# Performance work log

Hardware: AMD Instinct MI355X
Metric: run time of the kernel (lower is better)

Reference implementation:

```python
import jax, jax.numpy as jnp
import numpy as np

N_NODES = 50000
N_EDGES = 800000
D_IN = 256
D_OUT = 128


def setup_inputs() -> dict:
    key = jax.random.key(0)
    k1, k2, k3 = jax.random.split(key, 3)
    x = jax.random.normal(k1, (N_NODES, D_IN), dtype=jnp.float32)
    edge_index = jax.random.randint(k2, (2, N_EDGES), 0, N_NODES, dtype=jnp.int64)
    W = jax.random.normal(k3, (D_IN, D_OUT), dtype=jnp.float32) / np.sqrt(D_IN)
    b = jnp.zeros((D_OUT,), dtype=jnp.float32)
    prelu_a = jnp.full((D_OUT,), 0.25, dtype=jnp.float32)  # PyTorch PReLU default init
    return {"x": x, "edge_index": edge_index, "W": W, "b": b, "prelu_a": prelu_a}


def reference(x, edge_index, W, b, prelu_a):
    N = x.shape[0]
    # GCNConv default: add self-loops, symmetric deg^{-1/2} normalization
    self_loops = jnp.arange(N, dtype=edge_index.dtype)
    src = jnp.concatenate([edge_index[0], self_loops])  # message source j
    dst = jnp.concatenate([edge_index[1], self_loops])  # aggregation target i
    deg = jax.ops.segment_sum(jnp.ones_like(dst, dtype=x.dtype), dst, num_segments=N)
    dinv = jnp.where(deg > 0, jax.lax.rsqrt(deg), 0.0)
    norm = dinv[src] * dinv[dst]  # [E+N]
    h = x @ W  # [N, D_OUT] linear transform before aggregation
    msg = h[src] * norm[:, None]  # gather + scale
    out = jax.ops.segment_sum(msg, dst, num_segments=N) + b  # scatter-add + bias
    # per-channel PReLU
    return jnp.where(out > 0, out, prelu_a * out)
```

## Files before the change

kernel.cpp:

```cpp
#include <hip/hip_runtime.h>

#define N_NODES 50000
#define N_EDGES 800000
#define D_IN    256
#define D_OUT   128
#define ELL_S   64
#define PART_BLKS 391
#define GEMM_BLKS 391
#define NBINS   196
#define EPB     2048
#define CAPB    40

typedef __attribute__((ext_vector_type(8))) short short8;
typedef __attribute__((ext_vector_type(4))) float floatx4;

__device__ __forceinline__ unsigned short f2bf(float f) {
    unsigned int u = __float_as_uint(f);
    unsigned int r = (u + 0x7fffu + ((u >> 16) & 1u)) >> 16;
    return (unsigned short)r;
}
__device__ __forceinline__ unsigned int pack2(float a, float b) {
    return (unsigned int)f2bf(a) | ((unsigned int)f2bf(b) << 16);
}
__device__ __forceinline__ float bfl(unsigned int u) { return __uint_as_float(u << 16); }
__device__ __forceinline__ float bfh(unsigned int u) { return __uint_as_float(u & 0xffff0000u); }

__global__ __launch_bounds__(256) void fused_kernel(const float* __restrict__ x,
                                                    const float* __restrict__ W,
                                                    const void* __restrict__ ei,
                                                    int* __restrict__ packed,
                                                    int* __restrict__ blkBinCnt,
                                                    unsigned short* __restrict__ h) {
    __shared__ unsigned short As[128][40];
    __shared__ unsigned short bLds[4096 * 8];
    __shared__ int hist[NBINS];
    __shared__ int found32;
    const int bid = blockIdx.x;
    const int tid = threadIdx.x;

    if (bid < PART_BLKS) {
        int sb = bid;
        if (tid < NBINS) hist[tid] = 0;
        if (tid == 0) found32 = 0;
        __syncthreads();
        {
            const unsigned int* e32 = (const unsigned int*)ei;
            if (e32[2 * tid + 1] != 0u) atomicOr(&found32, 1);
        }
        __syncthreads();
        int is64 = !found32;

        int ebase = sb * EPB + tid;
        int sv[8], bn[8], dl[8], lr[8];
        if (is64) {
            const long long* p = (const long long*)ei;
#pragma unroll
            for (int i = 0; i < 8; i++) {
                int e = ebase + i * 256;
                if (e < N_EDGES) {
                    sv[i] = (int)p[e];
                    int d = (int)p[N_EDGES + e];
                    bn[i] = d >> 8; dl[i] = d & 255;
                } else bn[i] = -1;
            }
        } else {
            const int* p = (const int*)ei;
#pragma unroll
            for (int i = 0; i < 8; i++) {
                int e = ebase + i * 256;
                if (e < N_EDGES) {
                    sv[i] = p[e];
                    int d = p[N_EDGES + e];
                    bn[i] = d >> 8; dl[i] = d & 255;
                } else bn[i] = -1;
            }
        }
#pragma unroll
        for (int i = 0; i < 8; i++)
            if (bn[i] >= 0) lr[i] = atomicAdd(&hist[bn[i]], 1);
#pragma unroll
        for (int i = 0; i < 8; i++) {
            if (bn[i] >= 0 && lr[i] < CAPB)
                packed[((size_t)sb * NBINS + bn[i]) * CAPB + lr[i]] = sv[i] | (dl[i] << 24);
        }
        __syncthreads();
        for (int t = tid; t < NBINS; t += 256)
            blkBinCnt[sb * NBINS + t] = hist[t];
        return;
    }

#pragma unroll
    for (int seg = 0; seg < 16; seg++) {
        int g = seg * 256 + tid;
        int gl = g & 63;
        int kc = (g >> 6) & 7;
        int ct = g >> 9;
        int n  = ct * 16 + (gl & 15);
        int kb = kc * 32 + ((gl >> 4) & 3) * 8;
        unsigned int p[4];
#pragma unroll
        for (int jj = 0; jj < 4; jj++) {
            float a = W[(size_t)(kb + 2 * jj + 0) * D_OUT + n];
            float b = W[(size_t)(kb + 2 * jj + 1) * D_OUT + n];
            p[jj] = pack2(a, b);
        }
        *(uint4*)&bLds[(size_t)g * 8] = make_uint4(p[0], p[1], p[2], p[3]);
    }

    int row0 = (bid - PART_BLKS) * 128;
    int w    = tid >> 6;
    int lane = tid & 63;
    int quad = lane >> 4;
    int l15  = lane & 15;

    floatx4 acc[2][8];
#pragma unroll
    for (int i = 0; i < 2; i++)
#pragma unroll
        for (int j = 0; j < 8; j++) acc[i][j] = (floatx4){0.f, 0.f, 0.f, 0.f};

    int srow  = tid >> 1;
    int shalf = (tid & 1) * 16;
    const float* xrow = x + (size_t)(row0 + srow) * D_IN;
    bool svalid = (row0 + srow) < N_NODES;

    for (int k0 = 0; k0 < D_IN; k0 += 32) {
        uint4 p0 = make_uint4(0, 0, 0, 0), p1 = make_uint4(0, 0, 0, 0);
        if (svalid) {
            const float* src = xrow + k0 + shalf;
            float4 f0 = *(const float4*)(src + 0);
            float4 f1 = *(const float4*)(src + 4);
            float4 f2 = *(const float4*)(src + 8);
            float4 f3 = *(const float4*)(src + 12);
            p0 = make_uint4(pack2(f0.x, f0.y), pack2(f0.z, f0.w),
                            pack2(f1.x, f1.y), pack2(f1.z, f1.w));
            p1 = make_uint4(pack2(f2.x, f2.y), pack2(f2.z, f2.w),
                            pack2(f3.x, f3.y), pack2(f3.z, f3.w));
        }
        __syncthreads();
        *(uint4*)&As[srow][shalf + 0] = p0;
        *(uint4*)&As[srow][shalf + 8] = p1;
        __syncthreads();

        short8 a0 = *(const short8*)&As[w * 32 + l15][quad * 8];
        short8 a1 = *(const short8*)&As[w * 32 + 16 + l15][quad * 8];
        int kc = k0 >> 5;
#pragma unroll
        for (int ct = 0; ct < 8; ct++) {
            short8 b = *(const short8*)&bLds[(size_t)(((ct * 8 + kc) * 64 + lane)) * 8];
            acc[0][ct] = __builtin_amdgcn_mfma_f32_16x16x32_bf16(a0, b, acc[0][ct], 0, 0, 0);
            acc[1][ct] = __builtin_amdgcn_mfma_f32_16x16x32_bf16(a1, b, acc[1][ct], 0, 0, 0);
        }
    }

#pragma unroll
    for (int rt = 0; rt < 2; rt++) {
        int grow0 = row0 + w * 32 + rt * 16 + quad * 4;
#pragma unroll
        for (int r = 0; r < 4; r++) {
            int grow = grow0 + r;
            if (grow < N_NODES) {
#pragma unroll
                for (int ct = 0; ct < 8; ct++) {
                    h[(size_t)grow * D_OUT + ct * 16 + l15] = f2bf(acc[rt][ct][r]);
                }
            }
        }
    }
}

__global__ __launch_bounds__(256) void ell_kernel(const int* __restrict__ packed,
                                                  const int* __restrict__ blkBinCnt,
                                                  int* __restrict__ cnt,
                                                  int* __restrict__ bucket) {
    __shared__ int c256[256];
    int j = blockIdx.x, tid = threadIdx.x;
    c256[tid] = 0;
    __syncthreads();
    for (int sb = tid; sb < PART_BLKS; sb += 256) {
        int c = blkBinCnt[sb * NBINS + j];
        if (c > CAPB) c = CAPB;
        const int* seg = packed + ((size_t)sb * NBINS + j) * CAPB;
        for (int r = 0; r < c; ++r) {
            int rec = seg[r];
            int dl  = ((unsigned int)rec) >> 24;
            int s   = rec & 0xFFFFFF;
            int pos = atomicAdd(&c256[dl], 1);
            if (pos < ELL_S) bucket[(size_t)((j << 8) + dl) * ELL_S + pos] = s;
        }
    }
    __syncthreads();
    int d = (j << 8) + tid;
    if (d < N_NODES) cnt[d] = c256[tid];
}

#define GACC(U, F)                                      \
    a0 += bfl(U.x) * (F); a1 += bfh(U.x) * (F);         \
    a2 += bfl(U.y) * (F); a3 += bfh(U.y) * (F);         \
    a4 += bfl(U.z) * (F); a5 += bfh(U.z) * (F);         \
    a6 += bfl(U.w) * (F); a7 += bfh(U.w) * (F);

#define GBODY(SS, WW, KB)                                                         \
    {                                                                             \
        int lim = wave_max - (KB);                                                \
        if (lim > 16) lim = 16;                                                   \
        for (int k = 0; k < lim; k += 4) {                                        \
            int   s0 = __shfl((SS), gk + k + 0), s1 = __shfl((SS), gk + k + 1);   \
            int   s2 = __shfl((SS), gk + k + 2), s3 = __shfl((SS), gk + k + 3);   \
            float f0 = __shfl((WW), gk + k + 0), f1 = __shfl((WW), gk + k + 1);   \
            float f2 = __shfl((WW), gk + k + 2), f3 = __shfl((WW), gk + k + 3);   \
            uint4 u0 = *(const uint4*)(h + (size_t)s0 * D_OUT + co);              \
            uint4 u1 = *(const uint4*)(h + (size_t)s1 * D_OUT + co);              \
            uint4 u2 = *(const uint4*)(h + (size_t)s2 * D_OUT + co);              \
            uint4 u3 = *(const uint4*)(h + (size_t)s3 * D_OUT + co);              \
            GACC(u0, f0); GACC(u1, f1); GACC(u2, f2); GACC(u3, f3);               \
        }                                                                         \
    }

__global__ __launch_bounds__(256) void gather_kernel(
    const unsigned short* __restrict__ h, const int* __restrict__ cnt,
    const int* __restrict__ bucket, const float* __restrict__ bias,
    const float* __restrict__ pa, float* __restrict__ out) {
    int wave = (int)((blockIdx.x * blockDim.x + threadIdx.x) >> 6);
    int lane = threadIdx.x & 63;
    int g  = lane >> 4;
    int l  = lane & 15;
    int gk = g << 4;
    int d  = wave * 4 + g;
    if (wave >= N_NODES / 4) return;

    int nraw = cnt[d];
    int n = nraw < ELL_S ? nraw : ELL_S;
    float di = rsqrtf((float)(nraw + 1));

    int co = l * 8;

    uint4 us = *(const uint4*)(h + (size_t)d * D_OUT + co);
    float sl = di * di;
    float a0 = bfl(us.x) * sl, a1 = bfh(us.x) * sl;
    float a2 = bfl(us.y) * sl, a3 = bfh(us.y) * sl;
    float a4 = bfl(us.z) * sl, a5 = bfh(us.z) * sl;
    float a6 = bfl(us.w) * sl, a7 = bfh(us.w) * sl;

    int db = d * ELL_S;
    int   s0v = 0,   s1v = 0,   s2v = 0,   s3v = 0;
    float w0v = 0.f, w1v = 0.f, w2v = 0.f, w3v = 0.f;
    if (l      < n) { s0v = bucket[db + l];      w0v = rsqrtf((float)(cnt[s0v] + 1)) * di; }
    if (l + 16 < n) { s1v = bucket[db + l + 16]; w1v = rsqrtf((float)(cnt[s1v] + 1)) * di; }
    if (l + 32 < n) { s2v = bucket[db + l + 32]; w2v = rsqrtf((float)(cnt[s2v] + 1)) * di; }
    if (l + 48 < n) { s3v = bucket[db + l + 48]; w3v = rsqrtf((float)(cnt[s3v] + 1)) * di; }

    int wave_max = n;
    { int t = __shfl_xor(wave_max, 16); wave_max = t > wave_max ? t : wave_max; }
    { int t = __shfl_xor(wave_max, 32); wave_max = t > wave_max ? t : wave_max; }

    if (wave_max > 0)  GBODY(s0v, w0v, 0)
    if (wave_max > 16) GBODY(s1v, w1v, 16)
    if (wave_max > 32) GBODY(s2v, w2v, 32)
    if (wave_max > 48) GBODY(s3v, w3v, 48)

    int c = l * 8;
    float4 b0 = *(const float4*)&bias[c];
    float4 b1 = *(const float4*)&bias[c + 4];
    float4 p0 = *(const float4*)&pa[c];
    float4 p1 = *(const float4*)&pa[c + 4];
    float4 o0, o1;
    o0.x = a0 + b0.x; o0.y = a1 + b0.y; o0.z = a2 + b0.z; o0.w = a3 + b0.w;
    o1.x = a4 + b1.x; o1.y = a5 + b1.y; o1.z = a6 + b1.z; o1.w = a7 + b1.w;
    o0.x = o0.x > 0.f ? o0.x : p0.x * o0.x;
    o0.y = o0.y > 0.f ? o0.y : p0.y * o0.y;
    o0.z = o0.z > 0.f ? o0.z : p0.z * o0.z;
    o0.w = o0.w > 0.f ? o0.w : p0.w * o0.w;
    o1.x = o1.x > 0.f ? o1.x : p1.x * o1.x;
    o1.y = o1.y > 0.f ? o1.y : p1.y * o1.y;
    o1.z = o1.z > 0.f ? o1.z : p1.z * o1.z;
    o1.w = o1.w > 0.f ? o1.w : p1.w * o1.w;
    *(float4*)&out[(size_t)d * D_OUT + c]     = o0;
    *(float4*)&out[(size_t)d * D_OUT + c + 4] = o1;
}

extern "C" void kernel_launch(void* const* d_in, const int* in_sizes, int n_in,
                              void* d_out, int out_size, void* d_ws, size_t ws_size,
                              hipStream_t stream) {
    const float* x  = (const float*)d_in[0];
    const void*  ei = d_in[1];
    const float* W  = (const float*)d_in[2];
    const float* b  = (const float*)d_in[3];
    const float* pa = (const float*)d_in[4];
    float* out = (float*)d_out;

    char* w = (char*)d_ws;
    int*   packed = (int*)w;    w += (size_t)PART_BLKS * NBINS * CAPB * 4;
    int*   bbc    = (int*)w;    w += (size_t)PART_BLKS * NBINS * 4;
    int*   cnt    = (int*)w;    w += (size_t)NBINS * 256 * 4;
    int*   bucket = (int*)w;    w += (size_t)N_NODES * ELL_S * 4;
    unsigned short* h = (unsigned short*)w; w += (size_t)N_NODES * D_OUT * 2;

    fused_kernel<<<PART_BLKS + GEMM_BLKS, 256, 0, stream>>>(x, W, ei, packed, bbc, h);
    ell_kernel<<<NBINS, 256, 0, stream>>>(packed, bbc, cnt, bucket);
    gather_kernel<<<(N_NODES / 4 * 64 + 255) / 256, 256, 0, stream>>>(h, cnt, bucket, b, pa, out);
}
```

Baseline: 170.0 us.

## Regroup stages: pack W once, overlap GEMM with ELL build, pipeline gather loads

The edge partition now shares a kernel with a one-time packing of W into bf16 MFMA fragments in global memory. The GEMM blocks then share a launch with the ELL bucket-building blocks, so the GEMM overlaps with bucket construction. This removes the 64KB per-block LDS copy of W, which may raise occupancy, and the GEMM now reads its B fragments straight from global/L2. The gather loop is rewritten as a fixed 16-wide software-pipelined section so more row loads are in flight, though it always does 16 shuffles/loads per section regardless of the actual count.

```diff
diff --git a/kernel.cpp b/kernel.cpp
--- a/kernel.cpp
+++ b/kernel.cpp
@@ -6,6 +6,7 @@
 #define D_OUT   128
 #define ELL_S   64
 #define PART_BLKS 391
+#define PACK_BLKS 16
 #define GEMM_BLKS 391
 #define NBINS   196
 #define EPB     2048
@@ -25,73 +26,18 @@
 __device__ __forceinline__ float bfl(unsigned int u) { return __uint_as_float(u << 16); }
 __device__ __forceinline__ float bfh(unsigned int u) { return __uint_as_float(u & 0xffff0000u); }
 
-__global__ __launch_bounds__(256) void fused_kernel(const float* __restrict__ x,
-                                                    const float* __restrict__ W,
-                                                    const void* __restrict__ ei,
-                                                    int* __restrict__ packed,
-                                                    int* __restrict__ blkBinCnt,
-                                                    unsigned short* __restrict__ h) {
-    __shared__ unsigned short As[128][40];
-    __shared__ unsigned short bLds[4096 * 8];
+__global__ __launch_bounds__(256) void part_kernel(const void* __restrict__ ei,
+                                                   const float* __restrict__ W,
+                                                   unsigned short* __restrict__ bfrag,
+                                                   int* __restrict__ packed,
+                                                   int* __restrict__ blkBinCnt) {
     __shared__ int hist[NBINS];
     __shared__ int found32;
     const int bid = blockIdx.x;
     const int tid = threadIdx.x;
 
-    if (bid < PART_BLKS) {
-        int sb = bid;
-        if (tid < NBINS) hist[tid] = 0;
-        if (tid == 0) found32 = 0;
-        __syncthreads();
-        {
-            const unsigned int* e32 = (const unsigned int*)ei;
-            if (e32[2 * tid + 1] != 0u) atomicOr(&found32, 1);
-        }
-        __syncthreads();
-        int is64 = !found32;
-
-        int ebase = sb * EPB + tid;
-        int sv[8], bn[8], dl[8], lr[8];
-        if (is64) {
-            const long long* p = (const long long*)ei;
-#pragma unroll
-            for (int i = 0; i < 8; i++) {
-                int e = ebase + i * 256;
-                if (e < N_EDGES) {
-                    sv[i] = (int)p[e];
-                    int d = (int)p[N_EDGES + e];
-                    bn[i] = d >> 8; dl[i] = d & 255;
-                } else bn[i] = -1;
-            }
-        } else {
-            const int* p = (const int*)ei;
-#pragma unroll
-            for (int i = 0; i < 8; i++) {
-                int e = ebase + i * 256;
-                if (e < N_EDGES) {
-                    sv[i] = p[e];
-                    int d = p[N_EDGES + e];
-                    bn[i] = d >> 8; dl[i] = d & 255;
-                } else bn[i] = -1;
-            }
-        }
-#pragma unroll
-        for (int i = 0; i < 8; i++)
-            if (bn[i] >= 0) lr[i] = atomicAdd(&hist[bn[i]], 1);
-#pragma unroll
-        for (int i = 0; i < 8; i++) {
-            if (bn[i] >= 0 && lr[i] < CAPB)
-                packed[((size_t)sb * NBINS + bn[i]) * CAPB + lr[i]] = sv[i] | (dl[i] << 24);
-        }
-        __syncthreads();
-        for (int t = tid; t < NBINS; t += 256)
-            blkBinCnt[sb * NBINS + t] = hist[t];
-        return;
-    }
-
-#pragma unroll
-    for (int seg = 0; seg < 16; seg++) {
-        int g = seg * 256 + tid;
+    if (bid >= PART_BLKS) {
+        int g = (bid - PART_BLKS) * 256 + tid;
         int gl = g & 63;
         int kc = (g >> 6) & 7;
         int ct = g >> 9;
@@ -104,10 +50,93 @@
             float b = W[(size_t)(kb + 2 * jj + 1) * D_OUT + n];
             p[jj] = pack2(a, b);
         }
-        *(uint4*)&bLds[(size_t)g * 8] = make_uint4(p[0], p[1], p[2], p[3]);
-    }
-
-    int row0 = (bid - PART_BLKS) * 128;
+        *(uint4*)&bfrag[(size_t)g * 8] = make_uint4(p[0], p[1], p[2], p[3]);
+        return;
+    }
+
+    int sb = bid;
+    if (tid < NBINS) hist[tid] = 0;
+    if (tid == 0) found32 = 0;
+    __syncthreads();
+    {
+        const unsigned int* e32 = (const unsigned int*)ei;
+        if (e32[2 * tid + 1] != 0u) atomicOr(&found32, 1);
+    }
+    __syncthreads();
+    int is64 = !found32;
+
+    int ebase = sb * EPB + tid;
+    int sv[8], bn[8], dl[8], lr[8];
+    if (is64) {
+        const long long* p = (const long long*)ei;
+#pragma unroll
+        for (int i = 0; i < 8; i++) {
+            int e = ebase + i * 256;
+            if (e < N_EDGES) {
+                sv[i] = (int)p[e];
+                int d = (int)p[N_EDGES + e];
+                bn[i] = d >> 8; dl[i] = d & 255;
+            } else bn[i] = -1;
+        }
+    } else {
+        const int* p = (const int*)ei;
+#pragma unroll
+        for (int i = 0; i < 8; i++) {
+            int e = ebase + i * 256;
+            if (e < N_EDGES) {
+                sv[i] = p[e];
+                int d = p[N_EDGES + e];
+                bn[i] = d >> 8; dl[i] = d & 255;
+            } else bn[i] = -1;
+        }
+    }
+#pragma unroll
+    for (int i = 0; i < 8; i++)
+        if (bn[i] >= 0) lr[i] = atomicAdd(&hist[bn[i]], 1);
+#pragma unroll
+    for (int i = 0; i < 8; i++) {
+        if (bn[i] >= 0 && lr[i] < CAPB)
+            packed[((size_t)sb * NBINS + bn[i]) * CAPB + lr[i]] = sv[i] | (dl[i] << 24);
+    }
+    __syncthreads();
+    for (int t = tid; t < NBINS; t += 256)
+        blkBinCnt[sb * NBINS + t] = hist[t];
+}
+
+__global__ __launch_bounds__(256) void fused_kernel(const float* __restrict__ x,
+                                                    const unsigned short* __restrict__ bf,
+                                                    unsigned short* __restrict__ h,
+                                                    const int* __restrict__ packed,
+                                                    const int* __restrict__ blkBinCnt,
+                                                    int* __restrict__ cnt,
+                                                    int* __restrict__ bucket) {
+    __shared__ unsigned short As[128][40];
+    __shared__ int c256[256];
+    int tid = threadIdx.x;
+
+    if (blockIdx.x >= GEMM_BLKS) {
+        int j = blockIdx.x - GEMM_BLKS;
+        c256[tid] = 0;
+        __syncthreads();
+        for (int sb = tid; sb < PART_BLKS; sb += 256) {
+            int c = blkBinCnt[sb * NBINS + j];
+            if (c > CAPB) c = CAPB;
+            const int* seg = packed + ((size_t)sb * NBINS + j) * CAPB;
+            for (int r = 0; r < c; ++r) {
+                int rec = seg[r];
+                int dl  = ((unsigned int)rec) >> 24;
+                int s   = rec & 0xFFFFFF;
+                int pos = atomicAdd(&c256[dl], 1);
+                if (pos < ELL_S) bucket[(size_t)((j << 8) + dl) * ELL_S + pos] = s;
+            }
+        }
+        __syncthreads();
+        int d = (j << 8) + tid;
+        if (d < N_NODES) cnt[d] = c256[tid];
+        return;
+    }
+
+    int row0 = blockIdx.x * 128;
     int w    = tid >> 6;
     int lane = tid & 63;
     int quad = lane >> 4;
@@ -147,7 +176,7 @@
         int kc = k0 >> 5;
 #pragma unroll
         for (int ct = 0; ct < 8; ct++) {
-            short8 b = *(const short8*)&bLds[(size_t)(((ct * 8 + kc) * 64 + lane)) * 8];
+            short8 b = *(const short8*)&bf[(size_t)(((ct * 8 + kc) * 64 + lane)) * 8];
             acc[0][ct] = __builtin_amdgcn_mfma_f32_16x16x32_bf16(a0, b, acc[0][ct], 0, 0, 0);
             acc[1][ct] = __builtin_amdgcn_mfma_f32_16x16x32_bf16(a1, b, acc[1][ct], 0, 0, 0);
         }
@@ -167,31 +196,6 @@
             }
         }
     }
-}
-
-__global__ __launch_bounds__(256) void ell_kernel(const int* __restrict__ packed,
-                                                  const int* __restrict__ blkBinCnt,
-                                                  int* __restrict__ cnt,
-                                                  int* __restrict__ bucket) {
-    __shared__ int c256[256];
-    int j = blockIdx.x, tid = threadIdx.x;
-    c256[tid] = 0;
-    __syncthreads();
-    for (int sb = tid; sb < PART_BLKS; sb += 256) {
-        int c = blkBinCnt[sb * NBINS + j];
-        if (c > CAPB) c = CAPB;
-        const int* seg = packed + ((size_t)sb * NBINS + j) * CAPB;
-        for (int r = 0; r < c; ++r) {
-            int rec = seg[r];
-            int dl  = ((unsigned int)rec) >> 24;
-            int s   = rec & 0xFFFFFF;
-            int pos = atomicAdd(&c256[dl], 1);
-            if (pos < ELL_S) bucket[(size_t)((j << 8) + dl) * ELL_S + pos] = s;
-        }
-    }
-    __syncthreads();
-    int d = (j << 8) + tid;
-    if (d < N_NODES) cnt[d] = c256[tid];
 }
 
 #define GACC(U, F)                                      \
@@ -200,21 +204,32 @@
     a4 += bfl(U.z) * (F); a5 += bfh(U.z) * (F);         \
     a6 += bfl(U.w) * (F); a7 += bfh(U.w) * (F);
 
-#define GBODY(SS, WW, KB)                                                         \
-    {                                                                             \
-        int lim = wave_max - (KB);                                                \
-        if (lim > 16) lim = 16;                                                   \
-        for (int k = 0; k < lim; k += 4) {                                        \
-            int   s0 = __shfl((SS), gk + k + 0), s1 = __shfl((SS), gk + k + 1);   \
-            int   s2 = __shfl((SS), gk + k + 2), s3 = __shfl((SS), gk + k + 3);   \
-            float f0 = __shfl((WW), gk + k + 0), f1 = __shfl((WW), gk + k + 1);   \
-            float f2 = __shfl((WW), gk + k + 2), f3 = __shfl((WW), gk + k + 3);   \
-            uint4 u0 = *(const uint4*)(h + (size_t)s0 * D_OUT + co);              \
-            uint4 u1 = *(const uint4*)(h + (size_t)s1 * D_OUT + co);              \
-            uint4 u2 = *(const uint4*)(h + (size_t)s2 * D_OUT + co);              \
-            uint4 u3 = *(const uint4*)(h + (size_t)s3 * D_OUT + co);              \
-            GACC(u0, f0); GACC(u1, f1); GACC(u2, f2); GACC(u3, f3);               \
-        }                                                                         \
+#define SHL(SS, WW, KK, SV, FV)                         \
+    SV = __shfl((SS), gk + (KK)); FV = __shfl((WW), gk + (KK));
+#define LD4(SV, UV)                                     \
+    UV = *(const uint4*)(h + (size_t)(SV) * D_OUT + co);
+
+#define SEC(SS, WW)                                                          \
+    {                                                                        \
+        int   t0, t1, t2, t3, t4, t5, t6, t7;                                \
+        float f0, f1, f2, f3, f4, f5, f6, f7;                                \
+        uint4 u0, u1, u2, u3, u4, u5, u6, u7;                                \
+        SHL(SS, WW, 0, t0, f0) SHL(SS, WW, 1, t1, f1)                        \
+        SHL(SS, WW, 2, t2, f2) SHL(SS, WW, 3, t3, f3)                        \
+        LD4(t0, u0) LD4(t1, u1) LD4(t2, u2) LD4(t3, u3)                      \
+        SHL(SS, WW, 4, t4, f4) SHL(SS, WW, 5, t5, f5)                        \
+        SHL(SS, WW, 6, t6, f6) SHL(SS, WW, 7, t7, f7)                        \
+        LD4(t4, u4) LD4(t5, u5) LD4(t6, u6) LD4(t7, u7)                      \
+        GACC(u0, f0) GACC(u1, f1) GACC(u2, f2) GACC(u3, f3)                  \
+        SHL(SS, WW, 8, t0, f0) SHL(SS, WW, 9, t1, f1)                        \
+        SHL(SS, WW, 10, t2, f2) SHL(SS, WW, 11, t3, f3)                      \
+        LD4(t0, u0) LD4(t1, u1) LD4(t2, u2) LD4(t3, u3)                      \
+        GACC(u4, f4) GACC(u5, f5) GACC(u6, f6) GACC(u7, f7)                  \
+        SHL(SS, WW, 12, t4, f4) SHL(SS, WW, 13, t5, f5)                      \
+        SHL(SS, WW, 14, t6, f6) SHL(SS, WW, 15, t7, f7)                      \
+        LD4(t4, u4) LD4(t5, u5) LD4(t6, u6) LD4(t7, u7)                      \
+        GACC(u0, f0) GACC(u1, f1) GACC(u2, f2) GACC(u3, f3)                  \
+        GACC(u4, f4) GACC(u5, f5) GACC(u6, f6) GACC(u7, f7)                  \
     }
 
 __global__ __launch_bounds__(256) void gather_kernel(
@@ -254,10 +269,10 @@
     { int t = __shfl_xor(wave_max, 16); wave_max = t > wave_max ? t : wave_max; }
     { int t = __shfl_xor(wave_max, 32); wave_max = t > wave_max ? t : wave_max; }
 
-    if (wave_max > 0)  GBODY(s0v, w0v, 0)
-    if (wave_max > 16) GBODY(s1v, w1v, 16)
-    if (wave_max > 32) GBODY(s2v, w2v, 32)
-    if (wave_max > 48) GBODY(s3v, w3v, 48)
+    if (wave_max > 0)  SEC(s0v, w0v)
+    if (wave_max > 16) SEC(s1v, w1v)
+    if (wave_max > 32) SEC(s2v, w2v)
+    if (wave_max > 48) SEC(s3v, w3v)
 
     int c = l * 8;
     float4 b0 = *(const float4*)&bias[c];
@@ -290,13 +305,14 @@
     float* out = (float*)d_out;
 
     char* w = (char*)d_ws;
+    unsigned short* bfrag = (unsigned short*)w; w += 8 * 8 * 64 * 8 * 2;
     int*   packed = (int*)w;    w += (size_t)PART_BLKS * NBINS * CAPB * 4;
     int*   bbc    = (int*)w;    w += (size_t)PART_BLKS * NBINS * 4;
     int*   cnt    = (int*)w;    w += (size_t)NBINS * 256 * 4;
     int*   bucket = (int*)w;    w += (size_t)N_NODES * ELL_S * 4;
     unsigned short* h = (unsigned short*)w; w += (size_t)N_NODES * D_OUT * 2;
 
-    fused_kernel<<<PART_BLKS + GEMM_BLKS, 256, 0, stream>>>(x, W, ei, packed, bbc, h);
-    ell_kernel<<<NBINS, 256, 0, stream>>>(packed, bbc, cnt, bucket);
+    part_kernel<<<PART_BLKS + PACK_BLKS, 256, 0, stream>>>(ei, W, bfrag, packed, bbc);
+    fused_kernel<<<GEMM_BLKS + NBINS, 256, 0, stream>>>(x, bfrag, h, packed, bbc, cnt, bucket);
     gather_kernel<<<(N_NODES / 4 * 64 + 255) / 256, 256, 0, stream>>>(h, cnt, bucket, b, pa, out);
 }
```

Result: no change. 170.6 us (+0.4%).

## Regroup kernels: overlap ELL build with GEMM, pre-pack W fragments globally

Applied to the files above, without the earlier changes.

Splits work differently across launches. Edge partitioning and a one-time bf16 packing of W into MFMA fragment order run together in the first kernel. The GEMM then runs concurrently with the ELL bucket build in the second kernel. GEMM blocks no longer each repack W into 64KB of LDS and instead read the pre-packed fragments from global memory (cache). This cuts LDS use and raises occupancy, but adds global loads on the MFMA path. The gather loop bound changes from a wave-wide max to a per-group count rounded up to four.

```diff
diff --git a/kernel.cpp b/kernel.cpp
--- a/kernel.cpp
+++ b/kernel.cpp
@@ -6,6 +6,7 @@
 #define D_OUT   128
 #define ELL_S   64
 #define PART_BLKS 391
+#define PACK_BLKS 16
 #define GEMM_BLKS 391
 #define NBINS   196
 #define EPB     2048
@@ -25,73 +26,18 @@
 __device__ __forceinline__ float bfl(unsigned int u) { return __uint_as_float(u << 16); }
 __device__ __forceinline__ float bfh(unsigned int u) { return __uint_as_float(u & 0xffff0000u); }
 
-__global__ __launch_bounds__(256) void fused_kernel(const float* __restrict__ x,
-                                                    const float* __restrict__ W,
-                                                    const void* __restrict__ ei,
-                                                    int* __restrict__ packed,
-                                                    int* __restrict__ blkBinCnt,
-                                                    unsigned short* __restrict__ h) {
-    __shared__ unsigned short As[128][40];
-    __shared__ unsigned short bLds[4096 * 8];
+__global__ __launch_bounds__(256) void part_kernel(const void* __restrict__ ei,
+                                                   const float* __restrict__ W,
+                                                   unsigned short* __restrict__ bfrag,
+                                                   int* __restrict__ packed,
+                                                   int* __restrict__ blkBinCnt) {
     __shared__ int hist[NBINS];
     __shared__ int found32;
     const int bid = blockIdx.x;
     const int tid = threadIdx.x;
 
-    if (bid < PART_BLKS) {
-        int sb = bid;
-        if (tid < NBINS) hist[tid] = 0;
-        if (tid == 0) found32 = 0;
-        __syncthreads();
-        {
-            const unsigned int* e32 = (const unsigned int*)ei;
-            if (e32[2 * tid + 1] != 0u) atomicOr(&found32, 1);
-        }
-        __syncthreads();
-        int is64 = !found32;
-
-        int ebase = sb * EPB + tid;
-        int sv[8], bn[8], dl[8], lr[8];
-        if (is64) {
-            const long long* p = (const long long*)ei;
-#pragma unroll
-            for (int i = 0; i < 8; i++) {
-                int e = ebase + i * 256;
-                if (e < N_EDGES) {
-                    sv[i] = (int)p[e];
-                    int d = (int)p[N_EDGES + e];
-                    bn[i] = d >> 8; dl[i] = d & 255;
-                } else bn[i] = -1;
-            }
-        } else {
-            const int* p = (const int*)ei;
-#pragma unroll
-            for (int i = 0; i < 8; i++) {
-                int e = ebase + i * 256;
-                if (e < N_EDGES) {
-                    sv[i] = p[e];
-                    int d = p[N_EDGES + e];
-                    bn[i] = d >> 8; dl[i] = d & 255;
-                } else bn[i] = -1;
-            }
-        }
-#pragma unroll
-        for (int i = 0; i < 8; i++)
-            if (bn[i] >= 0) lr[i] = atomicAdd(&hist[bn[i]], 1);
-#pragma unroll
-        for (int i = 0; i < 8; i++) {
-            if (bn[i] >= 0 && lr[i] < CAPB)
-                packed[((size_t)sb * NBINS + bn[i]) * CAPB + lr[i]] = sv[i] | (dl[i] << 24);
-        }
-        __syncthreads();
-        for (int t = tid; t < NBINS; t += 256)
-            blkBinCnt[sb * NBINS + t] = hist[t];
-        return;
-    }
-
-#pragma unroll
-    for (int seg = 0; seg < 16; seg++) {
-        int g = seg * 256 + tid;
+    if (bid >= PART_BLKS) {
+        int g = (bid - PART_BLKS) * 256 + tid;
         int gl = g & 63;
         int kc = (g >> 6) & 7;
         int ct = g >> 9;
@@ -104,10 +50,93 @@
             float b = W[(size_t)(kb + 2 * jj + 1) * D_OUT + n];
             p[jj] = pack2(a, b);
         }
-        *(uint4*)&bLds[(size_t)g * 8] = make_uint4(p[0], p[1], p[2], p[3]);
-    }
-
-    int row0 = (bid - PART_BLKS) * 128;
+        *(uint4*)&bfrag[(size_t)g * 8] = make_uint4(p[0], p[1], p[2], p[3]);
+        return;
+    }
+
+    int sb = bid;
+    if (tid < NBINS) hist[tid] = 0;
+    if (tid == 0) found32 = 0;
+    __syncthreads();
+    {
+        const unsigned int* e32 = (const unsigned int*)ei;
+        if (e32[2 * tid + 1] != 0u) atomicOr(&found32, 1);
+    }
+    __syncthreads();
+    int is64 = !found32;
+
+    int ebase = sb * EPB + tid;
+    int sv[8], bn[8], dl[8], lr[8];
+    if (is64) {
+        const long long* p = (const long long*)ei;
+#pragma unroll
+        for (int i = 0; i < 8; i++) {
+            int e = ebase + i * 256;
+            if (e < N_EDGES) {
+                sv[i] = (int)p[e];
+                int d = (int)p[N_EDGES + e];
+                bn[i] = d >> 8; dl[i] = d & 255;
+            } else bn[i] = -1;
+        }
+    } else {
+        const int* p = (const int*)ei;
+#pragma unroll
+        for (int i = 0; i < 8; i++) {
+            int e = ebase + i * 256;
+            if (e < N_EDGES) {
+                sv[i] = p[e];
+                int d = p[N_EDGES + e];
+                bn[i] = d >> 8; dl[i] = d & 255;
+            } else bn[i] = -1;
+        }
+    }
+#pragma unroll
+    for (int i = 0; i < 8; i++)
+        if (bn[i] >= 0) lr[i] = atomicAdd(&hist[bn[i]], 1);
+#pragma unroll
+    for (int i = 0; i < 8; i++) {
+        if (bn[i] >= 0 && lr[i] < CAPB)
+            packed[((size_t)sb * NBINS + bn[i]) * CAPB + lr[i]] = sv[i] | (dl[i] << 24);
+    }
+    __syncthreads();
+    for (int t = tid; t < NBINS; t += 256)
+        blkBinCnt[sb * NBINS + t] = hist[t];
+}
+
+__global__ __launch_bounds__(256) void fused_kernel(const float* __restrict__ x,
+                                                    const unsigned short* __restrict__ bf,
+                                                    unsigned short* __restrict__ h,
+                                                    const int* __restrict__ packed,
+                                                    const int* __restrict__ blkBinCnt,
+                                                    int* __restrict__ cnt,
+                                                    int* __restrict__ bucket) {
+    __shared__ unsigned short As[128][40];
+    __shared__ int c256[256];
+    int tid = threadIdx.x;
+
+    if (blockIdx.x >= GEMM_BLKS) {
+        int j = blockIdx.x - GEMM_BLKS;
+        c256[tid] = 0;
+        __syncthreads();
+        for (int sb = tid; sb < PART_BLKS; sb += 256) {
+            int c = blkBinCnt[sb * NBINS + j];
+            if (c > CAPB) c = CAPB;
+            const int* seg = packed + ((size_t)sb * NBINS + j) * CAPB;
+            for (int r = 0; r < c; ++r) {
+                int rec = seg[r];
+                int dl  = ((unsigned int)rec) >> 24;
+                int s   = rec & 0xFFFFFF;
+                int pos = atomicAdd(&c256[dl], 1);
+                if (pos < ELL_S) bucket[(size_t)((j << 8) + dl) * ELL_S + pos] = s;
+            }
+        }
+        __syncthreads();
+        int d = (j << 8) + tid;
+        if (d < N_NODES) cnt[d] = c256[tid];
+        return;
+    }
+
+    int row0 = blockIdx.x * 128;
     int w    = tid >> 6;
     int lane = tid & 63;
     int quad = lane >> 4;
@@ -147,7 +176,7 @@
         int kc = k0 >> 5;
 #pragma unroll
         for (int ct = 0; ct < 8; ct++) {
-            short8 b = *(const short8*)&bLds[(size_t)(((ct * 8 + kc) * 64 + lane)) * 8];
+            short8 b = *(const short8*)&bf[(size_t)(((ct * 8 + kc) * 64 + lane)) * 8];
             acc[0][ct] = __builtin_amdgcn_mfma_f32_16x16x32_bf16(a0, b, acc[0][ct], 0, 0, 0);
             acc[1][ct] = __builtin_amdgcn_mfma_f32_16x16x32_bf16(a1, b, acc[1][ct], 0, 0, 0);
         }
@@ -167,31 +196,6 @@
             }
         }
     }
-}
-
-__global__ __launch_bounds__(256) void ell_kernel(const int* __restrict__ packed,
-                                                  const int* __restrict__ blkBinCnt,
-                                                  int* __restrict__ cnt,
-                                                  int* __restrict__ bucket) {
-    __shared__ int c256[256];
-    int j = blockIdx.x, tid = threadIdx.x;
-    c256[tid] = 0;
-    __syncthreads();
-    for (int sb = tid; sb < PART_BLKS; sb += 256) {
-        int c = blkBinCnt[sb * NBINS + j];
-        if (c > CAPB) c = CAPB;
-        const int* seg = packed + ((size_t)sb * NBINS + j) * CAPB;
-        for (int r = 0; r < c; ++r) {
-            int rec = seg[r];
-            int dl  = ((unsigned int)rec) >> 24;
-            int s   = rec & 0xFFFFFF;
-            int pos = atomicAdd(&c256[dl], 1);
-            if (pos < ELL_S) bucket[(size_t)((j << 8) + dl) * ELL_S + pos] = s;
-        }
-    }
-    __syncthreads();
-    int d = (j << 8) + tid;
-    if (d < N_NODES) cnt[d] = c256[tid];
 }
 
 #define GACC(U, F)                                      \
@@ -202,8 +206,9 @@
 
 #define GBODY(SS, WW, KB)                                                         \
     {                                                                             \
-        int lim = wave_max - (KB);                                                \
+        int lim = n - (KB);                                                       \
         if (lim > 16) lim = 16;                                                   \
+        lim = (lim + 3) & ~3;                                                     \
         for (int k = 0; k < lim; k += 4) {                                        \
             int   s0 = __shfl((SS), gk + k + 0), s1 = __shfl((SS), gk + k + 1);   \
             int   s2 = __shfl((SS), gk + k + 2), s3 = __shfl((SS), gk + k + 3);   \
@@ -231,6 +236,7 @@
 
     int nraw = cnt[d];
     int n = nraw < ELL_S ? nraw : ELL_S;
+    if (n < 0) n = 0;
     float di = rsqrtf((float)(nraw + 1));
 
     int co = l * 8;
@@ -250,14 +256,10 @@
     if (l + 32 < n) { s2v = bucket[db + l + 32]; w2v = rsqrtf((float)(cnt[s2v] + 1)) * di; }
     if (l + 48 < n) { s3v = bucket[db + l + 48]; w3v = rsqrtf((float)(cnt[s3v] + 1)) * di; }
 
-    int wave_max = n;
-    { int t = __shfl_xor(wave_max, 16); wave_max = t > wave_max ? t : wave_max; }
-    { int t = __shfl_xor(wave_max, 32); wave_max = t > wave_max ? t : wave_max; }
-
-    if (wave_max > 0)  GBODY(s0v, w0v, 0)
-    if (wave_max > 16) GBODY(s1v, w1v, 16)
-    if (wave_max > 32) GBODY(s2v, w2v, 32)
-    if (wave_max > 48) GBODY(s3v, w3v, 48)
+    if (n > 0)  GBODY(s0v, w0v, 0)
+    if (n > 16) GBODY(s1v, w1v, 16)
+    if (n > 32) GBODY(s2v, w2v, 32)
+    if (n > 48) GBODY(s3v, w3v, 48)
 
     int c = l * 8;
     float4 b0 = *(const float4*)&bias[c];
@@ -290,13 +292,14 @@
     float* out = (float*)d_out;
 
     char* w = (char*)d_ws;
+    unsigned short* bfrag = (unsigned short*)w; w += 8 * 8 * 64 * 8 * 2;
     int*   packed = (int*)w;    w += (size_t)PART_BLKS * NBINS * CAPB * 4;
     int*   bbc    = (int*)w;    w += (size_t)PART_BLKS * NBINS * 4;
     int*   cnt    = (int*)w;    w += (size_t)NBINS * 256 * 4;
     int*   bucket = (int*)w;    w += (size_t)N_NODES * ELL_S * 4;
     unsigned short* h = (unsigned short*)w; w += (size_t)N_NODES * D_OUT * 2;
 
-    fused_kernel<<<PART_BLKS + GEMM_BLKS, 256, 0, stream>>>(x, W, ei, packed, bbc, h);
-    ell_kernel<<<NBINS, 256, 0, stream>>>(packed, bbc, cnt, bucket);
+    part_kernel<<<PART_BLKS + PACK_BLKS, 256, 0, stream>>>(ei, W, bfrag, packed, bbc);
+    fused_kernel<<<GEMM_BLKS + NBINS, 256, 0, stream>>>(x, bfrag, h, packed, bbc, cnt, bucket);
     gather_kernel<<<(N_NODES / 4 * 64 + 255) / 256, 256, 0, stream>>>(h, cnt, bucket, b, pa, out);
 }
```

After: 172.8 us. Within noise of the previous version (+1.7%).
